# Optimization experiments

Hardware: AMD Instinct MI355X
Metric: run time of the kernel (lower is better)

## Reference

```python
import jax, jax.numpy as jnp
import numpy as np

H = 512
NH = 8  # num attention heads
HD = H // NH


def lstm_scan(x_seq, Wih, Whh, bih, bhh, reverse=False, h0=None, c0=None):
    """x_seq: [T, B, D] -> outputs [T, B, Hdim] (PyTorch gate order i,f,g,o)."""
    Hdim = Whh.shape[1]
    B = x_seq.shape[1]
    if h0 is None:
        h0 = jnp.zeros((B, Hdim), x_seq.dtype)
        c0 = jnp.zeros((B, Hdim), x_seq.dtype)
    # precompute input contributions for all timesteps (one big GEMM)
    xg = x_seq @ Wih.T + bih + bhh  # [T, B, 4H]

    def step(carry, xg_t):
        h, c = carry
        gates = xg_t + h @ Whh.T
        i, f, g, o = jnp.split(gates, 4, axis=-1)
        c = jax.nn.sigmoid(f) * c + jax.nn.sigmoid(i) * jnp.tanh(g)
        h = jax.nn.sigmoid(o) * jnp.tanh(c)
        return (h, c), h

    _, hs = jax.lax.scan(step, (h0, c0), xg, reverse=reverse)
    return hs


def mha(q_in, kv_in, in_w, in_b, out_w, out_b):
    """PyTorch-style MultiheadAttention (batch_first). q_in [B,Tq,H], kv_in [B,Tk,H]."""
    Wq, Wk, Wv = jnp.split(in_w, 3, axis=0)
    bq, bk, bv = jnp.split(in_b, 3, axis=0)
    B, Tq, _ = q_in.shape
    Tk = kv_in.shape[1]
    q = (q_in @ Wq.T + bq).reshape(B, Tq, NH, HD)
    k = (kv_in @ Wk.T + bk).reshape(B, Tk, NH, HD)
    v = (kv_in @ Wv.T + bv).reshape(B, Tk, NH, HD)
    scores = jnp.einsum('bqhd,bkhd->bhqk', q, k) / jnp.sqrt(jnp.array(HD, q.dtype))
    attn = jax.nn.softmax(scores, axis=-1)
    out = jnp.einsum('bhqk,bkhd->bqhd', attn, v).reshape(B, Tq, H)
    return out @ out_w.T + out_b


def setup_inputs() -> dict:
    key = jax.random.key(0)
    ks = jax.random.split(key, 32)
    B, T_txt, T_mel, V, M = 16, 256, 400, 256, 80
    s = 0.05
    inp = {
        'phoneme_indices': jax.random.randint(ks[0], (B, T_txt), 0, V),
        'mel_specs': jax.random.normal(ks[1], (B, T_mel, M), jnp.float32),
        'emb': jax.random.normal(ks[2], (V, H)) * s,
        'enc_f_Wih': jax.random.normal(ks[3], (4 * H, H)) * s,
        'enc_f_Whh': jax.random.normal(ks[4], (4 * H, H)) * s,
        'enc_f_bih': jax.random.normal(ks[5], (4 * H,)) * s,
        'enc_f_bhh': jax.random.normal(ks[6], (4 * H,)) * s,
        'enc_b_Wih': jax.random.normal(ks[7], (4 * H, H)) * s,
        'enc_b_Whh': jax.random.normal(ks[8], (4 * H, H)) * s,
        'enc_b_bih': jax.random.normal(ks[9], (4 * H,)) * s,
        'enc_b_bhh': jax.random.normal(ks[10], (4 * H,)) * s,
        'tp_W': jax.random.normal(ks[11], (H, 2 * H)) * s,
        'tp_b': jax.random.normal(ks[12], (H,)) * s,
        'mpi_W': jax.random.normal(ks[13], (H, M)) * s,
        'mpi_b': jax.random.normal(ks[14], (H,)) * s,
        'attn_in_w': jax.random.normal(ks[15], (3 * H, H)) * s,
        'attn_in_b': jax.random.normal(ks[16], (3 * H,)) * s,
        'attn_out_w': jax.random.normal(ks[17], (H, H)) * s,
        'attn_out_b': jax.random.normal(ks[18], (H,)) * s,
        'dec_Wih': jax.random.normal(ks[19], (4 * H, 2 * H)) * s,
        'dec_Whh': jax.random.normal(ks[20], (4 * H, H)) * s,
        'dec_bih': jax.random.normal(ks[21], (4 * H,)) * s,
        'dec_bhh': jax.random.normal(ks[22], (4 * H,)) * s,
        'mpo_W': jax.random.normal(ks[23], (M, H)) * s,
        'mpo_b': jax.random.normal(ks[24], (M,)) * s,
    }
    return inp


def reference(phoneme_indices, mel_specs, emb,
              enc_f_Wih, enc_f_Whh, enc_f_bih, enc_f_bhh,
              enc_b_Wih, enc_b_Whh, enc_b_bih, enc_b_bhh,
              tp_W, tp_b, mpi_W, mpi_b,
              attn_in_w, attn_in_b, attn_out_w, attn_out_b,
              dec_Wih, dec_Whh, dec_bih, dec_bhh, mpo_W, mpo_b):
    # ---- encode_text (dropout = identity in eval mode) ----
    x = emb[phoneme_indices]                       # [B, Ttxt, H]
    x_t = jnp.transpose(x, (1, 0, 2))              # [Ttxt, B, H]
    h_f = lstm_scan(x_t, enc_f_Wih, enc_f_Whh, enc_f_bih, enc_f_bhh)
    h_b = lstm_scan(x_t, enc_b_Wih, enc_b_Whh, enc_b_bih, enc_b_bhh, reverse=True)
    text_encoded = jnp.concatenate([h_f, h_b], axis=-1)          # [Ttxt, B, 2H]
    text_encoded = jnp.transpose(text_encoded, (1, 0, 2)) @ tp_W.T + tp_b  # [B, Ttxt, H]

    # ---- teacher-forced decoder inputs: shift mel right, prepend zeros ----
    B, T_mel, M = mel_specs.shape
    mel_shifted = jnp.concatenate(
        [jnp.zeros((B, 1, M), mel_specs.dtype), mel_specs[:, :-1, :]], axis=1)
    mel_projected = mel_shifted @ mpi_W.T + mpi_b                # [B, Tmel, H]

    # cross-attention (queries independent of decoder state -> batched)
    attended = mha(mel_projected, text_encoded, attn_in_w, attn_in_b,
                   attn_out_w, attn_out_b)                       # [B, Tmel, H]

    decoder_input = jnp.concatenate([mel_projected, attended], axis=-1)  # [B, Tmel, 2H]
    dec_out = lstm_scan(jnp.transpose(decoder_input, (1, 0, 2)),
                        dec_Wih, dec_Whh, dec_bih, dec_bhh)      # [Tmel, B, H]
    dec_out = jnp.transpose(dec_out, (1, 0, 2))
    return dec_out @ mpo_W.T + mpo_b                              # [B, Tmel, M]
```

## Files before the change

### kernel.cpp

```cpp
#include <hip/hip_runtime.h>
#include <hip/hip_bf16.h>
#include <math.h>


typedef short s16;
typedef __attribute__((ext_vector_type(8))) short bf16x8;
typedef __attribute__((ext_vector_type(4))) short s16x4;
typedef __attribute__((ext_vector_type(4))) float f32x4;
typedef __attribute__((ext_vector_type(4))) unsigned u32x4;

#define DEV static __device__ __forceinline__

DEV float b2f(s16 v) {
    unsigned u = ((unsigned)(unsigned short)v) << 16;
    return __builtin_bit_cast(float, u);
}
DEV s16 f2b(float f) {
    unsigned u = __builtin_bit_cast(unsigned, f);
    return (s16)((u + 0x7fffu + ((u >> 16) & 1u)) >> 16);
}

DEV float sigm_f(float x) {
    return __builtin_amdgcn_rcpf(1.0f + __builtin_amdgcn_exp2f(-1.4426950408889634f * x));
}
DEV float tanh_f(float x) {
    float e = __builtin_amdgcn_exp2f(2.8853900817779268f * x);
    return 1.0f - 2.0f * __builtin_amdgcn_rcpf(e + 1.0f);
}

static const bf16x8 BZERO = {0,0,0,0,0,0,0,0};

__global__ __launch_bounds__(256) void cvt_k(
    const float* __restrict__ src, s16* __restrict__ dst, int n4)
{
    int i = blockIdx.x * 256 + threadIdx.x;
    if (i >= n4) return;
    float4 v = ((const float4*)src)[i];
    s16x4 o = { f2b(v.x), f2b(v.y), f2b(v.z), f2b(v.w) };
    *(s16x4*)(dst + 4 * (size_t)i) = o;
}

__global__ __launch_bounds__(256) void gemm_k(
    const s16* __restrict__ A, int lda,
    const s16* __restrict__ W, int ldw,
    const float* __restrict__ b1, const float* __restrict__ b2,
    s16* __restrict__ C, float* __restrict__ Cf, int ldc,
    int M, int N, int K, int perm_tmel)
{
    int tid = threadIdx.x;
    int w = tid >> 6, l = tid & 63;
    int lr = l & 15, lk = l >> 4;
    int m0 = blockIdx.x * 128 + (w >> 1) * 64;
    int n0 = blockIdx.y * 128 + (w & 1) * 64;

    f32x4 acc[4][4];
    #pragma unroll
    for (int i = 0; i < 4; i++)
        #pragma unroll
        for (int j = 0; j < 4; j++) acc[i][j] = (f32x4){0.f, 0.f, 0.f, 0.f};

    for (int kk = 0; kk < K; kk += 32) {
        int kb = kk + lk * 8;
        bool kok = (kb + 8) <= K;
        bf16x8 av[4], bv[4];
        #pragma unroll
        for (int mi = 0; mi < 4; mi++) {
            int arow = m0 + mi * 16 + lr;
            av[mi] = (arow < M && kok) ? *(const bf16x8*)(A + (size_t)arow * lda + kb) : BZERO;
        }
        #pragma unroll
        for (int ni = 0; ni < 4; ni++) {
            int wrow = n0 + ni * 16 + lr;
            bv[ni] = (wrow < N && kok) ? *(const bf16x8*)(W + (size_t)wrow * ldw + kb) : BZERO;
        }
        #pragma unroll
        for (int mi = 0; mi < 4; mi++)
            #pragma unroll
            for (int ni = 0; ni < 4; ni++)
                acc[mi][ni] = __builtin_amdgcn_mfma_f32_16x16x32_bf16(av[mi], bv[ni], acc[mi][ni], 0, 0, 0);
    }

    #pragma unroll
    for (int ni = 0; ni < 4; ni++) {
        int col = n0 + ni * 16 + lr;
        if (col >= N) continue;
        float bias = 0.f;
        if (b1) bias += b1[col];
        if (b2) bias += b2[col];
        #pragma unroll
        for (int mi = 0; mi < 4; mi++) {
            #pragma unroll
            for (int r = 0; r < 4; r++) {
                int row = m0 + mi * 16 + lk * 4 + r;
                if (row >= M) continue;
                float v = acc[mi][ni][r] + bias;
                size_t oidx;
                if (perm_tmel) {
                    int bb = row & 15, t = row >> 4;
                    oidx = ((size_t)bb * perm_tmel + t) * ldc + col;
                } else {
                    oidx = (size_t)row * ldc + col;
                }
                if (Cf) Cf[oidx] = v;
                else    C[oidx] = f2b(v);
            }
        }
    }
}

__global__ __launch_bounds__(256) void embed_k(
    const int* __restrict__ idx, const s16* __restrict__ emb, s16* __restrict__ x)
{
    int gid = blockIdx.x * 256 + threadIdx.x;
    int r = gid >> 6, cc = (gid & 63) * 8;
    int t = r >> 4, b = r & 15;
    int id = idx[b * 256 + t];
    *(bf16x8*)(x + (size_t)r * 512 + cc) = *(const bf16x8*)(emb + (size_t)id * 512 + cc);
}

__global__ __launch_bounds__(256) void melshift_k(
    const float* __restrict__ mel, s16* __restrict__ ms)
{
    int gid = blockIdx.x * 256 + threadIdx.x;
    if (gid >= 6400 * 20) return;
    int r = gid / 20, cc = (gid % 20) * 4;
    int t = r >> 4, b = r & 15;
    s16x4 o = {0, 0, 0, 0};
    if (t > 0) {
        float4 v = *(const float4*)(mel + ((size_t)b * 400 + (t - 1)) * 80 + cc);
        o = (s16x4){ f2b(v.x), f2b(v.y), f2b(v.z), f2b(v.w) };
    }
    *(s16x4*)(ms + (size_t)r * 80 + cc) = o;
}

__global__ __launch_bounds__(256, 1) void lstm_pers_k(
    const s16* __restrict__ Whh0, const s16* __restrict__ Whh1,
    const s16* __restrict__ xg0,  const s16* __restrict__ xg1,
    int rev0, int rev1, int T,
    unsigned* hxch, s16* hs, int hs_ld, int coff0, int coff1)
{
    int dir = blockIdx.x >> 3;
    int bb  = blockIdx.x & 7;
    int j0  = bb * 64;
    const s16* Whh = dir ? Whh1 : Whh0;
    const s16* xg  = dir ? xg1  : xg0;
    int rev        = dir ? rev1 : rev0;
    int coff       = dir ? coff1 : coff0;
    unsigned* hx   = hxch + (size_t)dir * 2 * 8192;

    int tid = threadIdx.x;
    int w = tid >> 6, l = tid & 63;
    int lr = l & 15, lk = l >> 4;

    __shared__ s16 h_lds[2][16 * 512];

    int u  = j0 + w * 16 + lr;
    int b0 = lk * 4;

    float cv[4] = {0.f, 0.f, 0.f, 0.f};

    bf16x8 wf[4][16];
    #pragma unroll
    for (int g = 0; g < 4; g++) {
        const s16* wr = Whh + (size_t)(g * 512 + u) * 512;
        #pragma unroll
        for (int kk = 0; kk < 16; kk++)
            wf[g][kk] = *(const bf16x8*)(wr + kk * 32 + lk * 8);
    }

    {
        char* lb0 = (char*)&h_lds[0][0];
        #pragma unroll
        for (int r = 0; r < 4; r++) {
            int row = b0 + r;
            *(s16*)(lb0 + row * 1024 + ((u * 2) ^ ((row & 7) << 4))) = 0;
        }
    }

    s16 xv[4][4];
    {
        int t0 = rev ? (T - 1) : 0;
        const s16* xb = xg + ((size_t)t0 * 16 + b0) * 2048 + u;
        #pragma unroll
        for (int r = 0; r < 4; r++)
            #pragma unroll
            for (int g = 0; g < 4; g++)
                xv[g][r] = xb[(size_t)r * 2048 + g * 512];
    }

    int bw = tid * 4;
    #define STRIPE(i) ((((i) >= bb) ? (i) + 1 : (i)) * 1024)

    for (int s = 0; s < T; s++) {
        int te = rev ? (T - 1 - s) : s;
        int p  = s & 1;

        const unsigned* rb = hx + (size_t)p * 8192;
        const unsigned* q0 = rb + STRIPE(0) + bw;
        const unsigned* q1 = rb + STRIPE(1) + bw;
        const unsigned* q2 = rb + STRIPE(2) + bw;
        const unsigned* q3 = rb + STRIPE(3) + bw;
        const unsigned* q4 = rb + STRIPE(4) + bw;
        const unsigned* q5 = rb + STRIPE(5) + bw;
        const unsigned* q6 = rb + STRIPE(6) + bw;
        u32x4 v0, v1, v2, v3, v4, v5, v6;
        const unsigned tgw = ((unsigned)s) << 16;
        for (;;) {
            asm volatile(
                "global_load_dwordx4 %0, %7, off sc1\n\t"
                "global_load_dwordx4 %1, %8, off sc1\n\t"
                "global_load_dwordx4 %2, %9, off sc1\n\t"
                "global_load_dwordx4 %3, %10, off sc1\n\t"
                "global_load_dwordx4 %4, %11, off sc1\n\t"
                "global_load_dwordx4 %5, %12, off sc1\n\t"
                "global_load_dwordx4 %6, %13, off sc1\n\t"
                "s_waitcnt vmcnt(0)"
                : "=&v"(v0), "=&v"(v1), "=&v"(v2), "=&v"(v3),
                  "=&v"(v4), "=&v"(v5), "=&v"(v6)
                : "v"(q0), "v"(q1), "v"(q2), "v"(q3), "v"(q4), "v"(q5), "v"(q6)
                : "memory");
            unsigned m = 0;
            #define CHK(vv) m |= (vv[0] ^ tgw) | (vv[1] ^ tgw) | \
                                 (vv[2] ^ tgw) | (vv[3] ^ tgw)
            CHK(v0); CHK(v1); CHK(v2); CHK(v3); CHK(v4); CHK(v5); CHK(v6);
            #undef CHK
            if ((m & 0xffff0000u) == 0) break;
        }

        s16 xn[4][4];
        bool havenext = (s + 1) < T;
        if (havenext) {
            int tn = rev ? (T - 2 - s) : (s + 1);
            const s16* xb = xg + ((size_t)tn * 16 + b0) * 2048 + u;
            #pragma unroll
            for (int r = 0; r < 4; r++)
                #pragma unroll
                for (int g = 0; g < 4; g++)
                    xn[g][r] = xb[(size_t)r * 2048 + g * 512];
        }

        {
            char* lb = (char*)&h_lds[p][0];
            int row0 = bw & 15;
            auto stg = [&](int gw, u32x4 vv) {
                int col2 = (gw >> 4) * 2;
                #pragma unroll
                for (int k2 = 0; k2 < 4; k2++) {
                    int row = row0 + k2;
                    *(s16*)(lb + row * 1024 + (col2 ^ ((row & 7) << 4))) =
                        (s16)(vv[k2] & 0xffffu);
                }
            };
            stg(STRIPE(0) + bw, v0); stg(STRIPE(1) + bw, v1);
            stg(STRIPE(2) + bw, v2); stg(STRIPE(3) + bw, v3);
            stg(STRIPE(4) + bw, v4); stg(STRIPE(5) + bw, v5);
            stg(STRIPE(6) + bw, v6);
        }
        __syncthreads();

        f32x4 acc[4];
        #pragma unroll
        for (int i = 0; i < 4; i++) acc[i] = (f32x4){0.f, 0.f, 0.f, 0.f};
        const char* lb = (const char*)&h_lds[p][0];
        #pragma unroll
        for (int kk = 0; kk < 16; kk++) {
            bf16x8 af = *(const bf16x8*)(lb + lr * 1024 +
                             (((kk * 32 + lk * 8) * 2) ^ ((lr & 7) << 4)));
            #pragma unroll
            for (int g = 0; g < 4; g++)
                acc[g] = __builtin_amdgcn_mfma_f32_16x16x32_bf16(af, wf[g][kk], acc[g], 0, 0, 0);
        }

        s16 h4[4];
        #pragma unroll
        for (int r = 0; r < 4; r++) {
            float i_ = sigm_f(acc[0][r] + b2f(xv[0][r]));
            float f_ = sigm_f(acc[1][r] + b2f(xv[1][r]));
            float g_ = tanh_f(acc[2][r] + b2f(xv[2][r]));
            float o_ = sigm_f(acc[3][r] + b2f(xv[3][r]));
            float cn = f_ * cv[r] + i_ * g_;
            cv[r] = cn;
            h4[r] = f2b(o_ * tanh_f(cn));
        }

        {
            unsigned ntag = ((unsigned)(s + 1)) << 16;
            unsigned long long tag2 =
                ((unsigned long long)ntag << 32) | (unsigned long long)ntag;
            unsigned long long w0 = tag2
                | ((unsigned long long)(unsigned short)h4[1] << 32)
                | (unsigned long long)(unsigned short)h4[0];
            unsigned long long w1 = tag2
                | ((unsigned long long)(unsigned short)h4[3] << 32)
                | (unsigned long long)(unsigned short)h4[2];
            unsigned* wb = hx + (size_t)((s + 1) & 1) * 8192;
            unsigned long long* dst = (unsigned long long*)(wb + (u * 16 + b0));
            __hip_atomic_store(dst,     w0, __ATOMIC_RELAXED, __HIP_MEMORY_SCOPE_AGENT);
            __hip_atomic_store(dst + 1, w1, __ATOMIC_RELAXED, __HIP_MEMORY_SCOPE_AGENT);
        }
        {
            char* nb = (char*)&h_lds[p ^ 1][0];
            #pragma unroll
            for (int r = 0; r < 4; r++) {
                int row = b0 + r;
                *(s16*)(nb + row * 1024 + ((u * 2) ^ ((row & 7) << 4))) = h4[r];
            }
        }
        #pragma unroll
        for (int r = 0; r < 4; r++)
            hs[((size_t)te * 16 + b0 + r) * hs_ld + coff + u] = h4[r];

        if (havenext) {
            #pragma unroll
            for (int g = 0; g < 4; g++)
                #pragma unroll
                for (int r = 0; r < 4; r++)
                    xv[g][r] = xn[g][r];
        }
    }
    #undef STRIPE
}

__global__ __launch_bounds__(256) void attn_k(
    const s16* __restrict__ Q, const s16* __restrict__ Kmat,
    const s16* __restrict__ V, s16* __restrict__ Ao)
{
    __shared__ float S[16][256];
    __shared__ s16  P[16][256];

    int tile = blockIdx.x, head = blockIdx.y, b = blockIdx.z;
    int tq0 = tile * 16;
    int tid = threadIdx.x;
    int w = tid >> 6, l = tid & 63;
    int lr = l & 15, lk = l >> 4;
    int hoff = head * 64;

    f32x4 sacc[4];
    #pragma unroll
    for (int i = 0; i < 4; i++) sacc[i] = (f32x4){0.f, 0.f, 0.f, 0.f};

    for (int kk = 0; kk < 64; kk += 32) {
        int kb = kk + lk * 8;
        bf16x8 qf = *(const bf16x8*)(Q + (size_t)((tq0 + lr) * 16 + b) * 512 + hoff + kb);
        #pragma unroll
        for (int nb = 0; nb < 4; nb++) {
            int tk = w * 64 + nb * 16 + lr;
            bf16x8 kf = *(const bf16x8*)(Kmat + (size_t)(tk * 16 + b) * 512 + hoff + kb);
            sacc[nb] = __builtin_amdgcn_mfma_f32_16x16x32_bf16(qf, kf, sacc[nb], 0, 0, 0);
        }
    }
    #pragma unroll
    for (int nb = 0; nb < 4; nb++)
        #pragma unroll
        for (int r = 0; r < 4; r++)
            S[lk * 4 + r][w * 64 + nb * 16 + lr] = sacc[nb][r] * 0.125f;
    __syncthreads();

    {
        int row = tid >> 4, sl = tid & 15;
        float m = -1e30f;
        #pragma unroll
        for (int ii = 0; ii < 16; ii++) m = fmaxf(m, S[row][sl + 16 * ii]);
        #pragma unroll
        for (int off = 1; off < 16; off <<= 1) m = fmaxf(m, __shfl_xor(m, off));
        float sum = 0.f;
        #pragma unroll
        for (int ii = 0; ii < 16; ii++) {
            float e = expf(S[row][sl + 16 * ii] - m);
            S[row][sl + 16 * ii] = e;
            sum += e;
        }
        #pragma unroll
        for (int off = 1; off < 16; off <<= 1) sum += __shfl_xor(sum, off);
        float inv = 1.f / sum;
        #pragma unroll
        for (int ii = 0; ii < 16; ii++)
            P[row][sl + 16 * ii] = f2b(S[row][sl + 16 * ii] * inv);
    }
    __syncthreads();

    f32x4 oacc = (f32x4){0.f, 0.f, 0.f, 0.f};
    for (int kk = 0; kk < 256; kk += 32) {
        int kb = kk + lk * 8;
        bf16x8 pf = *(const bf16x8*)(&P[lr][kb]);
        bf16x8 vf;
        #pragma unroll
        for (int jj = 0; jj < 8; jj++)
            vf[jj] = V[(size_t)((kb + jj) * 16 + b) * 512 + hoff + w * 16 + lr];
        oacc = __builtin_amdgcn_mfma_f32_16x16x32_bf16(pf, vf, oacc, 0, 0, 0);
    }
    #pragma unroll
    for (int r = 0; r < 4; r++)
        Ao[(size_t)((tq0 + lk * 4 + r) * 16 + b) * 512 + hoff + w * 16 + lr] = f2b(oacc[r]);
}

extern "C" void kernel_launch(void* const* d_in, const int* in_sizes, int n_in,
                              void* d_out, int out_size, void* d_ws, size_t ws_size,
                              hipStream_t stream)
{
    const int*   pidx = (const int*)d_in[0];
    const float* mel  = (const float*)d_in[1];
    const float* emb  = (const float*)d_in[2];
    const float* fWih = (const float*)d_in[3];
    const float* fWhh = (const float*)d_in[4];
    const float* fbih = (const float*)d_in[5];
    const float* fbhh = (const float*)d_in[6];
    const float* bWih = (const float*)d_in[7];
    const float* bWhh = (const float*)d_in[8];
    const float* bbih = (const float*)d_in[9];
    const float* bbhh = (const float*)d_in[10];
    const float* tpW  = (const float*)d_in[11];
    const float* tpb  = (const float*)d_in[12];
    const float* mpiW = (const float*)d_in[13];
    const float* mpib = (const float*)d_in[14];
    const float* aiw  = (const float*)d_in[15];
    const float* aib  = (const float*)d_in[16];
    const float* aow  = (const float*)d_in[17];
    const float* aob  = (const float*)d_in[18];
    const float* dWih = (const float*)d_in[19];
    const float* dWhh = (const float*)d_in[20];
    const float* dbih = (const float*)d_in[21];
    const float* dbhh = (const float*)d_in[22];
    const float* mpoW = (const float*)d_in[23];
    const float* mpob = (const float*)d_in[24];

    char* ws = (char*)d_ws;
    size_t off = 0;
    auto alloc = [&](size_t bytes) -> char* {
        char* p = ws + off;
        off = (off + bytes + 255) & ~(size_t)255;
        return p;
    };

    s16* emb_b  = (s16*)alloc((size_t)131072 * 2);
    s16* fWih_b = (s16*)alloc((size_t)1048576 * 2);
    s16* fWhh_b = (s16*)alloc((size_t)1048576 * 2);
    s16* bWih_b = (s16*)alloc((size_t)1048576 * 2);
    s16* bWhh_b = (s16*)alloc((size_t)1048576 * 2);
    s16* tpW_b  = (s16*)alloc((size_t)524288 * 2);
    s16* mpiW_b = (s16*)alloc((size_t)40960 * 2);
    s16* aiw_b  = (s16*)alloc((size_t)786432 * 2);
    s16* aow_b  = (s16*)alloc((size_t)262144 * 2);
    s16* dWih_b = (s16*)alloc((size_t)2097152 * 2);
    s16* dWhh_b = (s16*)alloc((size_t)1048576 * 2);
    s16* mpoW_b = (s16*)alloc((size_t)40960 * 2);

    char* xgreg = alloc((size_t)4096 * 2048 * 2 * 2);
    s16* xgf    = (s16*)xgreg;
    s16* xgb    = (s16*)(xgreg + (size_t)4096 * 2048 * 2);
    s16* xgd    = (s16*)xgreg;
    s16* dec_hs = (s16*)(xgreg + (size_t)6400 * 2048 * 2);

    char* xreg  = alloc((size_t)4096 * 512 * 2);
    s16* x      = (s16*)xreg;
    s16* mshift = (s16*)xreg;

    char* ereg  = alloc((size_t)4096 * 1024 * 2);
    s16* enc_hs = (s16*)ereg;
    s16* attno  = (s16*)ereg;

    s16* tenc   = (s16*)alloc((size_t)4096 * 512 * 2);
    s16* decin  = (s16*)alloc((size_t)6400 * 1024 * 2);
    s16* Qb     = (s16*)alloc((size_t)6400 * 512 * 2);
    s16* Kb     = (s16*)alloc((size_t)4096 * 512 * 2);
    s16* Vb     = (s16*)alloc((size_t)4096 * 512 * 2);

    unsigned* hx_e = (unsigned*)alloc((size_t)2 * 2 * 8192 * 4);
    unsigned* hx_d = (unsigned*)alloc((size_t)2 * 8192 * 4);

    hipMemsetAsync(hx_e, 0, (size_t)2 * 2 * 8192 * 4, stream);
    hipMemsetAsync(hx_d, 0, (size_t)2 * 8192 * 4, stream);

    auto cvt = [&](const float* src, s16* dst, int n) {
        int n4 = n / 4;
        cvt_k<<<(n4 + 255) / 256, 256, 0, stream>>>(src, dst, n4);
    };
    cvt(emb,  emb_b,  131072);
    cvt(fWih, fWih_b, 1048576);
    cvt(fWhh, fWhh_b, 1048576);
    cvt(bWih, bWih_b, 1048576);
    cvt(bWhh, bWhh_b, 1048576);
    cvt(tpW,  tpW_b,  524288);
    cvt(mpiW, mpiW_b, 40960);
    cvt(aiw,  aiw_b,  786432);
    cvt(aow,  aow_b,  262144);
    cvt(dWih, dWih_b, 2097152);
    cvt(dWhh, dWhh_b, 1048576);
    cvt(mpoW, mpoW_b, 40960);

    auto gemm = [&](const s16* A, int lda, const s16* W, int ldw,
                    const float* b1, const float* b2,
                    s16* C, float* Cf, int ldc, int M, int N, int K, int perm) {
        dim3 g((M + 127) / 128, (N + 127) / 128);
        gemm_k<<<g, 256, 0, stream>>>(A, lda, W, ldw, b1, b2, C, Cf, ldc, M, N, K, perm);
    };

    embed_k<<<1024, 256, 0, stream>>>(pidx, emb_b, x);

    gemm(x, 512, fWih_b, 512, fbih, fbhh, xgf, nullptr, 2048, 4096, 2048, 512, 0);
    gemm(x, 512, bWih_b, 512, bbih, bbhh, xgb, nullptr, 2048, 4096, 2048, 512, 0);

    lstm_pers_k<<<16, 256, 0, stream>>>(
        fWhh_b, bWhh_b, xgf, xgb, 0, 1, 256,
        hx_e, enc_hs, 1024, 0, 512);

    gemm(enc_hs, 1024, tpW_b, 1024, tpb, nullptr, tenc, nullptr, 512, 4096, 512, 1024, 0);

    melshift_k<<<500, 256, 0, stream>>>(mel, mshift);
    gemm(mshift, 80, mpiW_b, 80, mpib, nullptr, decin, nullptr, 1024, 6400, 512, 80, 0);

    gemm(decin, 1024, aiw_b,              512, aib,       nullptr, Qb, nullptr, 512, 6400, 512, 512, 0);
    gemm(tenc,  512,  aiw_b + 512 * 512,  512, aib + 512, nullptr, Kb, nullptr, 512, 4096, 512, 512, 0);
    gemm(tenc,  512,  aiw_b + 1024 * 512, 512, aib + 1024,nullptr, Vb, nullptr, 512, 4096, 512, 512, 0);

    attn_k<<<dim3(25, 8, 16), 256, 0, stream>>>(Qb, Kb, Vb, attno);

    gemm(attno, 512, aow_b, 512, aob, nullptr, decin + 512, nullptr, 1024, 6400, 512, 512, 0);

    gemm(decin, 1024, dWih_b, 1024, dbih, dbhh, xgd, nullptr, 2048, 6400, 2048, 1024, 0);

    lstm_pers_k<<<8, 256, 0, stream>>>(
        dWhh_b, dWhh_b, xgd, xgd, 0, 0, 400,
        hx_d, dec_hs, 512, 0, 0);

    gemm(dec_hs, 512, mpoW_b, 512, mpob, nullptr, nullptr, (float*)d_out, 80, 6400, 80, 512, 400);
}
```

Baseline: 2.140 ms.

## Add per-block sentinel flags to LSTM sync, defer hs stores, batch weight conversions

The persistent LSTM kernel now spins on a small array of per-block sentinel words instead of repeatedly polling the whole tagged h exchange buffer. Each block publishes its sentinel after a vmcnt wait and barrier. The hs output store is deferred by one step, and the next-step xg loads are double-buffered and issued after the barrier, taking them off the critical path. The twelve weight conversion launches are merged into one multi-segment kernel. In exchange, each step gains an extra barrier, a vmcnt drain and a sentinel round trip, which may lengthen the serial per-step latency.

```diff
diff --git a/kernel.cpp b/kernel.cpp
--- a/kernel.cpp
+++ b/kernel.cpp
@@ -30,14 +30,20 @@
 
 static const bf16x8 BZERO = {0,0,0,0,0,0,0,0};
 
-__global__ __launch_bounds__(256) void cvt_k(
-    const float* __restrict__ src, s16* __restrict__ dst, int n4)
+struct CvtSeg { const float* src; s16* dst; int n4; };
+struct CvtArgs { CvtSeg seg[12]; int blk_off[12]; };
+
+__global__ __launch_bounds__(256) void cvt_all_k(CvtArgs a)
 {
-    int i = blockIdx.x * 256 + threadIdx.x;
-    if (i >= n4) return;
-    float4 v = ((const float4*)src)[i];
+    int blk = blockIdx.x;
+    int si = 0;
+    #pragma unroll
+    for (int k = 1; k < 12; k++) si += (blk >= a.blk_off[k]) ? 1 : 0;
+    int i = (blk - a.blk_off[si]) * 256 + threadIdx.x;
+    if (i >= a.seg[si].n4) return;
+    float4 v = ((const float4*)a.seg[si].src)[i];
     s16x4 o = { f2b(v.x), f2b(v.y), f2b(v.z), f2b(v.w) };
-    *(s16x4*)(dst + 4 * (size_t)i) = o;
+    *(s16x4*)(a.seg[si].dst + 4 * (size_t)i) = o;
 }
 
 __global__ __launch_bounds__(256) void gemm_k(
@@ -137,7 +143,8 @@
     const s16* __restrict__ Whh0, const s16* __restrict__ Whh1,
     const s16* __restrict__ xg0,  const s16* __restrict__ xg1,
     int rev0, int rev1, int T,
-    unsigned* hxch, s16* hs, int hs_ld, int coff0, int coff1)
+    unsigned* hxch, unsigned* sent,
+    s16* hs, int hs_ld, int coff0, int coff1)
 {
     int dir = blockIdx.x >> 3;
     int bb  = blockIdx.x & 7;
@@ -147,6 +154,7 @@
     int rev        = dir ? rev1 : rev0;
     int coff       = dir ? coff1 : coff0;
     unsigned* hx   = hxch + (size_t)dir * 2 * 8192;
+    unsigned* sb   = sent + (size_t)dir * 16;
 
     int tid = threadIdx.x;
     int w = tid >> 6, l = tid & 63;
@@ -177,23 +185,73 @@
         }
     }
 
-    s16 xv[4][4];
+    s16 xva[4][4], xvb[4][4];
     {
-        int t0 = rev ? (T - 1) : 0;
-        const s16* xb = xg + ((size_t)t0 * 16 + b0) * 2048 + u;
+        int t0i = rev ? (T - 1) : 0;
+        const s16* xb = xg + ((size_t)t0i * 16 + b0) * 2048 + u;
         #pragma unroll
         for (int r = 0; r < 4; r++)
             #pragma unroll
             for (int g = 0; g < 4; g++)
-                xv[g][r] = xb[(size_t)r * 2048 + g * 512];
-    }
+                xva[g][r] = xb[(size_t)r * 2048 + g * 512];
+    }
+
+    s16 hprev[4] = {0, 0, 0, 0};
+    int teprev = 0;
 
     int bw = tid * 4;
     #define STRIPE(i) ((((i) >= bb) ? (i) + 1 : (i)) * 1024)
+
+    #define PISSUE(X0,X1,X2,X3,X4,X5,X6)                                    \
+        asm volatile(                                                       \
+            "global_load_dwordx4 %0, %7, off sc1\n\t"                       \
+            "global_load_dwordx4 %1, %8, off sc1\n\t"                       \
+            "global_load_dwordx4 %2, %9, off sc1\n\t"                       \
+            "global_load_dwordx4 %3, %10, off sc1\n\t"                      \
+            "global_load_dwordx4 %4, %11, off sc1\n\t"                      \
+            "global_load_dwordx4 %5, %12, off sc1\n\t"                      \
+            "global_load_dwordx4 %6, %13, off sc1\n\t"                      \
+            "s_waitcnt vmcnt(0)"                                            \
+            : "=&v"(X0), "=&v"(X1), "=&v"(X2), "=&v"(X3),                   \
+              "=&v"(X4), "=&v"(X5), "=&v"(X6)                               \
+            : "v"(q0), "v"(q1), "v"(q2), "v"(q3), "v"(q4), "v"(q5), "v"(q6) \
+            : "memory")
+
+    #define TAGOK(X0,X1,X2,X3,X4,X5,X6)                                     \
+        ((((X0[0]^tgw)|(X0[2]^tgw) | (X1[0]^tgw)|(X1[2]^tgw) |              \
+           (X2[0]^tgw)|(X2[2]^tgw) | (X3[0]^tgw)|(X3[2]^tgw) |              \
+           (X4[0]^tgw)|(X4[2]^tgw) | (X5[0]^tgw)|(X5[2]^tgw) |              \
+           (X6[0]^tgw)|(X6[2]^tgw)) & 0xffff0000u) == 0u)
 
     for (int s = 0; s < T; s++) {
         int te = rev ? (T - 1 - s) : s;
         int p  = s & 1;
+        bool odd = (s & 1) != 0;
+        const unsigned tgw = ((unsigned)s) << 16;
+
+        {
+            const unsigned* sp = sb + (size_t)p * 8;
+            for (;;) {
+                unsigned e0, e1, e2, e3, e4, e5, e6, e7;
+                asm volatile(
+                    "global_load_dword %0, %8, off sc1\n\t"
+                    "global_load_dword %1, %8, off offset:4 sc1\n\t"
+                    "global_load_dword %2, %8, off offset:8 sc1\n\t"
+                    "global_load_dword %3, %8, off offset:12 sc1\n\t"
+                    "global_load_dword %4, %8, off offset:16 sc1\n\t"
+                    "global_load_dword %5, %8, off offset:20 sc1\n\t"
+                    "global_load_dword %6, %8, off offset:24 sc1\n\t"
+                    "global_load_dword %7, %8, off offset:28 sc1\n\t"
+                    "s_waitcnt vmcnt(0)"
+                    : "=&v"(e0), "=&v"(e1), "=&v"(e2), "=&v"(e3),
+                      "=&v"(e4), "=&v"(e5), "=&v"(e6), "=&v"(e7)
+                    : "v"(sp) : "memory");
+                __builtin_amdgcn_sched_barrier(0);
+                unsigned m = (e0 ^ tgw) | (e1 ^ tgw) | (e2 ^ tgw) | (e3 ^ tgw) |
+                             (e4 ^ tgw) | (e5 ^ tgw) | (e6 ^ tgw) | (e7 ^ tgw);
+                if (m == 0u) break;
+            }
+        }
 
         const unsigned* rb = hx + (size_t)p * 8192;
         const unsigned* q0 = rb + STRIPE(0) + bw;
@@ -203,41 +261,11 @@
         const unsigned* q4 = rb + STRIPE(4) + bw;
         const unsigned* q5 = rb + STRIPE(5) + bw;
         const unsigned* q6 = rb + STRIPE(6) + bw;
-        u32x4 v0, v1, v2, v3, v4, v5, v6;
-        const unsigned tgw = ((unsigned)s) << 16;
-        for (;;) {
-            asm volatile(
-                "global_load_dwordx4 %0, %7, off sc1\n\t"
-                "global_load_dwordx4 %1, %8, off sc1\n\t"
-                "global_load_dwordx4 %2, %9, off sc1\n\t"
-                "global_load_dwordx4 %3, %10, off sc1\n\t"
-                "global_load_dwordx4 %4, %11, off sc1\n\t"
-                "global_load_dwordx4 %5, %12, off sc1\n\t"
-                "global_load_dwordx4 %6, %13, off sc1\n\t"
-                "s_waitcnt vmcnt(0)"
-                : "=&v"(v0), "=&v"(v1), "=&v"(v2), "=&v"(v3),
-                  "=&v"(v4), "=&v"(v5), "=&v"(v6)
-                : "v"(q0), "v"(q1), "v"(q2), "v"(q3), "v"(q4), "v"(q5), "v"(q6)
-                : "memory");
-            unsigned m = 0;
-            #define CHK(vv) m |= (vv[0] ^ tgw) | (vv[1] ^ tgw) | \
-                                 (vv[2] ^ tgw) | (vv[3] ^ tgw)
-            CHK(v0); CHK(v1); CHK(v2); CHK(v3); CHK(v4); CHK(v5); CHK(v6);
-            #undef CHK
-            if ((m & 0xffff0000u) == 0) break;
-        }
-
-        s16 xn[4][4];
-        bool havenext = (s + 1) < T;
-        if (havenext) {
-            int tn = rev ? (T - 2 - s) : (s + 1);
-            const s16* xb = xg + ((size_t)tn * 16 + b0) * 2048 + u;
-            #pragma unroll
-            for (int r = 0; r < 4; r++)
-                #pragma unroll
-                for (int g = 0; g < 4; g++)
-                    xn[g][r] = xb[(size_t)r * 2048 + g * 512];
-        }
+        u32x4 A0, A1, A2, A3, A4, A5, A6;
+        do {
+            PISSUE(A0, A1, A2, A3, A4, A5, A6);
+            __builtin_amdgcn_sched_barrier(0);
+        } while (!TAGOK(A0, A1, A2, A3, A4, A5, A6));
 
         {
             char* lb = (char*)&h_lds[p][0];
@@ -251,12 +279,35 @@
                         (s16)(vv[k2] & 0xffffu);
                 }
             };
-            stg(STRIPE(0) + bw, v0); stg(STRIPE(1) + bw, v1);
-            stg(STRIPE(2) + bw, v2); stg(STRIPE(3) + bw, v3);
-            stg(STRIPE(4) + bw, v4); stg(STRIPE(5) + bw, v5);
-            stg(STRIPE(6) + bw, v6);
+            stg(STRIPE(0) + bw, A0); stg(STRIPE(1) + bw, A1);
+            stg(STRIPE(2) + bw, A2); stg(STRIPE(3) + bw, A3);
+            stg(STRIPE(4) + bw, A4); stg(STRIPE(5) + bw, A5);
+            stg(STRIPE(6) + bw, A6);
         }
         __syncthreads();
+
+        if (s > 0) {
+            #pragma unroll
+            for (int r = 0; r < 4; r++)
+                hs[((size_t)teprev * 16 + b0 + r) * hs_ld + coff + u] = hprev[r];
+        }
+        if (s + 1 < T) {
+            int tn = rev ? (T - 2 - s) : (s + 1);
+            const s16* xb = xg + ((size_t)tn * 16 + b0) * 2048 + u;
+            if (odd) {
+                #pragma unroll
+                for (int r = 0; r < 4; r++)
+                    #pragma unroll
+                    for (int g = 0; g < 4; g++)
+                        xva[g][r] = xb[(size_t)r * 2048 + g * 512];
+            } else {
+                #pragma unroll
+                for (int r = 0; r < 4; r++)
+                    #pragma unroll
+                    for (int g = 0; g < 4; g++)
+                        xvb[g][r] = xb[(size_t)r * 2048 + g * 512];
+            }
+        }
 
         f32x4 acc[4];
         #pragma unroll
@@ -274,10 +325,14 @@
         s16 h4[4];
         #pragma unroll
         for (int r = 0; r < 4; r++) {
-            float i_ = sigm_f(acc[0][r] + b2f(xv[0][r]));
-            float f_ = sigm_f(acc[1][r] + b2f(xv[1][r]));
-            float g_ = tanh_f(acc[2][r] + b2f(xv[2][r]));
-            float o_ = sigm_f(acc[3][r] + b2f(xv[3][r]));
+            float xi = b2f(odd ? xvb[0][r] : xva[0][r]);
+            float xf = b2f(odd ? xvb[1][r] : xva[1][r]);
+            float xgg = b2f(odd ? xvb[2][r] : xva[2][r]);
+            float xo = b2f(odd ? xvb[3][r] : xva[3][r]);
+            float i_ = sigm_f(acc[0][r] + xi);
+            float f_ = sigm_f(acc[1][r] + xf);
+            float g_ = tanh_f(acc[2][r] + xgg);
+            float o_ = sigm_f(acc[3][r] + xo);
             float cn = f_ * cv[r] + i_ * g_;
             cv[r] = cn;
             h4[r] = f2b(o_ * tanh_f(cn));
@@ -298,6 +353,16 @@
             __hip_atomic_store(dst,     w0, __ATOMIC_RELAXED, __HIP_MEMORY_SCOPE_AGENT);
             __hip_atomic_store(dst + 1, w1, __ATOMIC_RELAXED, __HIP_MEMORY_SCOPE_AGENT);
         }
+
+        asm volatile("s_waitcnt vmcnt(0)" ::: "memory");
+        __syncthreads();
+
+        if (tid == 0) {
+            __hip_atomic_store(&sb[(size_t)((s + 1) & 1) * 8 + bb],
+                               ((unsigned)(s + 1)) << 16,
+                               __ATOMIC_RELAXED, __HIP_MEMORY_SCOPE_AGENT);
+        }
+
         {
             char* nb = (char*)&h_lds[p ^ 1][0];
             #pragma unroll
@@ -306,19 +371,19 @@
                 *(s16*)(nb + row * 1024 + ((u * 2) ^ ((row & 7) << 4))) = h4[r];
             }
         }
-        #pragma unroll
-        for (int r = 0; r < 4; r++)
-            hs[((size_t)te * 16 + b0 + r) * hs_ld + coff + u] = h4[r];
-
-        if (havenext) {
-            #pragma unroll
-            for (int g = 0; g < 4; g++)
-                #pragma unroll
-                for (int r = 0; r < 4; r++)
-                    xv[g][r] = xn[g][r];
-        }
-    }
+
+        #pragma unroll
+        for (int r = 0; r < 4; r++) hprev[r] = h4[r];
+        teprev = te;
+    }
+
+    #pragma unroll
+    for (int r = 0; r < 4; r++)
+        hs[((size_t)teprev * 16 + b0 + r) * hs_ld + coff + u] = hprev[r];
+
     #undef STRIPE
+    #undef PISSUE
+    #undef TAGOK
 }
 
 __global__ __launch_bounds__(256) void attn_k(
@@ -468,25 +533,38 @@
     unsigned* hx_e = (unsigned*)alloc((size_t)2 * 2 * 8192 * 4);
     unsigned* hx_d = (unsigned*)alloc((size_t)2 * 8192 * 4);
 
+    unsigned* sent_e = (unsigned*)alloc(256);
+    unsigned* sent_d = (unsigned*)alloc(256);
+
     hipMemsetAsync(hx_e, 0, (size_t)2 * 2 * 8192 * 4, stream);
     hipMemsetAsync(hx_d, 0, (size_t)2 * 8192 * 4, stream);
-
-    auto cvt = [&](const float* src, s16* dst, int n) {
-        int n4 = n / 4;
-        cvt_k<<<(n4 + 255) / 256, 256, 0, stream>>>(src, dst, n4);
-    };
-    cvt(emb,  emb_b,  131072);
-    cvt(fWih, fWih_b, 1048576);
-    cvt(fWhh, fWhh_b, 1048576);
-    cvt(bWih, bWih_b, 1048576);
-    cvt(bWhh, bWhh_b, 1048576);
-    cvt(tpW,  tpW_b,  524288);
-    cvt(mpiW, mpiW_b, 40960);
-    cvt(aiw,  aiw_b,  786432);
-    cvt(aow,  aow_b,  262144);
-    cvt(dWih, dWih_b, 2097152);
-    cvt(dWhh, dWhh_b, 1048576);
-    cvt(mpoW, mpoW_b, 40960);
+    hipMemsetAsync(sent_e, 0, 128, stream);
+    hipMemsetAsync(sent_d, 0, 64, stream);
+
+    {
+        CvtArgs ca;
+        int boff = 0;
+        int i = 0;
+        auto addseg = [&](const float* s, s16* d, int n) {
+            ca.seg[i].src = s; ca.seg[i].dst = d; ca.seg[i].n4 = n / 4;
+            ca.blk_off[i] = boff;
+            boff += (n / 4 + 255) / 256;
+            i++;
+        };
+        addseg(emb,  emb_b,  131072);
+        addseg(fWih, fWih_b, 1048576);
+        addseg(fWhh, fWhh_b, 1048576);
+        addseg(bWih, bWih_b, 1048576);
+        addseg(bWhh, bWhh_b, 1048576);
+        addseg(tpW,  tpW_b,  524288);
+        addseg(mpiW, mpiW_b, 40960);
+        addseg(aiw,  aiw_b,  786432);
+        addseg(aow,  aow_b,  262144);
+        addseg(dWih, dWih_b, 2097152);
+        addseg(dWhh, dWhh_b, 1048576);
+        addseg(mpoW, mpoW_b, 40960);
+        cvt_all_k<<<boff, 256, 0, stream>>>(ca);
+    }
 
     auto gemm = [&](const s16* A, int lda, const s16* W, int ldw,
                     const float* b1, const float* b2,
@@ -502,7 +580,7 @@
 
     lstm_pers_k<<<16, 256, 0, stream>>>(
         fWhh_b, bWhh_b, xgf, xgb, 0, 1, 256,
-        hx_e, enc_hs, 1024, 0, 512);
+        hx_e, sent_e, enc_hs, 1024, 0, 512);
 
     gemm(enc_hs, 1024, tpW_b, 1024, tpb, nullptr, tenc, nullptr, 512, 4096, 512, 1024, 0);
 
@@ -521,7 +599,7 @@
 
     lstm_pers_k<<<8, 256, 0, stream>>>(
         dWhh_b, dWhh_b, xgd, xgd, 0, 0, 400,
-        hx_d, dec_hs, 512, 0, 0);
+        hx_d, sent_d, dec_hs, 512, 0, 0);
 
     gemm(dec_hs, 512, mpoW_b, 512, mpob, nullptr, nullptr, (float*)d_out, 80, 6400, 80, 512, 400);
 }
```

New measurement: 3.293 ms. +53.8%, slower.
